# Kernel optimization log

Measured on AMD Instinct MI355X. Metric: run time of the kernel, lower is better.

The kernel has to match this reference:

```python
import jax, jax.numpy as jnp
import numpy as np

DIM = 2048
N_HEAD = 32
N_KV_HEAD = 8
HEAD_DIM = DIM // N_HEAD  # 64
BSZ = 2
SEQ = 2048


def apply_rotary_emb(x, freqs_cis):
    # x: [b, s, h, d]; freqs_cis: [s, d//2, 2]
    xs = x.reshape(*x.shape[:-1], -1, 2)          # [b, s, h, d//2, 2]
    fc = freqs_cis.reshape(1, xs.shape[1], 1, xs.shape[3], 2)
    x0, x1 = xs[..., 0], xs[..., 1]
    c, s = fc[..., 0], fc[..., 1]
    out = jnp.stack([x0 * c - x1 * s, x1 * c + x0 * s], axis=-1)
    return out.reshape(x.shape).astype(x.dtype)


def setup_inputs() -> dict:
    key = jax.random.key(0)
    k1, k2, k3, k4 = jax.random.split(key, 4)
    x = jax.random.normal(k1, (BSZ, SEQ, DIM), dtype=jnp.float32)
    # rotary cos/sin table [seq, head_dim//2, 2]
    theta = 1.0 / (10000.0 ** (jnp.arange(0, HEAD_DIM, 2, dtype=jnp.float32) / HEAD_DIM))
    ang = jnp.arange(SEQ, dtype=jnp.float32)[:, None] * theta[None, :]
    freqs_cis = jnp.stack([jnp.cos(ang), jnp.sin(ang)], axis=-1)
    mask = jnp.tril(jnp.ones((SEQ, SEQ), dtype=bool))  # causal
    scale = 0.02
    wqkv = jax.random.normal(k2, ((N_HEAD + 2 * N_KV_HEAD) * HEAD_DIM, DIM), dtype=jnp.float32) * scale
    wo = jax.random.normal(k3, (DIM, DIM), dtype=jnp.float32) * scale
    return {"x": x, "freqs_cis": freqs_cis, "mask": mask, "wqkv": wqkv, "wo": wo}


def reference(x, freqs_cis, mask, wqkv, wo):
    bsz, seqlen, _ = x.shape
    kv_size = N_KV_HEAD * HEAD_DIM
    qkv = x @ wqkv.T  # [b, s, dim + 2*kv]
    xq, xk, xv = jnp.split(qkv, [DIM, DIM + kv_size], axis=-1)
    xq = xq.reshape(bsz, seqlen, N_HEAD, HEAD_DIM)
    xk = xk.reshape(bsz, seqlen, N_KV_HEAD, HEAD_DIM)
    xv = xv.reshape(bsz, seqlen, N_KV_HEAD, HEAD_DIM)
    xq = apply_rotary_emb(xq, freqs_cis)
    xk = apply_rotary_emb(xk, freqs_cis)
    # [b, h, s, d]
    xq = xq.transpose(0, 2, 1, 3)
    xk = xk.transpose(0, 2, 1, 3)
    xv = xv.transpose(0, 2, 1, 3)
    rep = N_HEAD // N_KV_HEAD
    keys = jnp.repeat(xk, rep, axis=1)
    values = jnp.repeat(xv, rep, axis=1)
    scores = jnp.einsum("bhqd,bhkd->bhqk", xq, keys) / np.sqrt(HEAD_DIM).astype(np.float32)
    scores = jnp.where(mask, scores, jnp.finfo(scores.dtype).min)
    attn = jax.nn.softmax(scores, axis=-1)
    out = jnp.einsum("bhqk,bhkd->bhqd", attn, values)
    out = out.transpose(0, 2, 1, 3).reshape(bsz, seqlen, DIM)
    return out @ wo.T
```

## Files before the change

kernel.cpp:

```cpp
#include <hip/hip_runtime.h>
#include <hip/hip_bf16.h>

typedef __attribute__((ext_vector_type(8))) short short8;
typedef __attribute__((ext_vector_type(4))) short short4v;
typedef __attribute__((ext_vector_type(4))) float f32x4;
typedef __hip_bfloat16 bf16;

#define SEQ 2048
#define DIM 2048
#define NH 32
#define NKV 8
#define HD 64
#define QKVD 3072
#define KVD 512
#define SMSCALE 0.18033688011112042f

__device__ inline void gld_lds16(const bf16* g, bf16* l) {
    __builtin_amdgcn_global_load_lds((const __attribute__((address_space(1))) void*)g,
                                     (__attribute__((address_space(3))) void*)l, 16, 0, 0);
}

__device__ inline void store_val(float* p, float v) { *p = v; }
__device__ inline void store_val(bf16* p, float v) { *p = __float2bfloat16(v); }

__device__ inline unsigned pkbf16(float a, float b) {
    __hip_bfloat162 h = __float22bfloat162_rn(make_float2(a, b));
    return *(unsigned*)&h;
}

__global__ void cvt3_kernel(const float* __restrict__ x, const float* __restrict__ wqkv,
                            const float* __restrict__ wo, bf16* __restrict__ out) {
    int i = blockIdx.x * blockDim.x + threadIdx.x;
    const float* src; int off;
    if (i < 2097152) { src = x; off = i; }
    else if (i < 3670016) { src = wqkv; off = i - 2097152; }
    else { src = wo; off = i - 3670016; }
    float4 v = ((const float4*)src)[off];
    uint2 u;
    u.x = pkbf16(v.x, v.y);
    u.y = pkbf16(v.z, v.w);
    ((uint2*)out)[i] = u;
}

template <typename CT>
__global__ __launch_bounds__(256, 3) void gemm_nt(const bf16* __restrict__ A,
                                                  const bf16* __restrict__ Bt,
                                                  CT* __restrict__ C,
                                                  int M, int N, int K) {
    __shared__ bf16 As[128 * 32];
    __shared__ bf16 Bs[128 * 32];
    const int tid = threadIdx.x;
    const int lane = tid & 63;
    const int quad = lane >> 4;
    const int r16 = lane & 15;
    const int wave = tid >> 6;
    const int bm = blockIdx.y * 128;
    const int bn = blockIdx.x * 128;
    const int wm = (wave >> 1) * 64;
    const int wn = (wave & 1) * 64;

    f32x4 acc[4][4] = {};

    const int arow = tid >> 2;
    const int kch = (tid & 3) * 8;
    const bf16* Ap = A + (size_t)(bm + arow) * K + kch;
    const bf16* Bp = Bt + (size_t)(bn + arow) * K + kch;
    bf16* Asd = As + tid * 8;
    bf16* Bsd = Bs + tid * 8;
    const int kq = quad * 8;

    for (int k0 = 0; k0 < K; k0 += 32) {
        __syncthreads();
        gld_lds16(Ap, Asd);
        gld_lds16(Ap + (size_t)64 * K, Asd + 64 * 32);
        gld_lds16(Bp, Bsd);
        gld_lds16(Bp + (size_t)64 * K, Bsd + 64 * 32);
        Ap += 32; Bp += 32;
        __syncthreads();
        short8 af[4], bfr[4];
#pragma unroll
        for (int i = 0; i < 4; i++)
            af[i] = *(const short8*)(As + (wm + i * 16 + r16) * 32 + kq);
#pragma unroll
        for (int j = 0; j < 4; j++)
            bfr[j] = *(const short8*)(Bs + (wn + j * 16 + r16) * 32 + kq);
#pragma unroll
        for (int i = 0; i < 4; i++)
#pragma unroll
            for (int j = 0; j < 4; j++)
                acc[i][j] = __builtin_amdgcn_mfma_f32_16x16x32_bf16(af[i], bfr[j], acc[i][j], 0, 0, 0);
    }
#pragma unroll
    for (int i = 0; i < 4; i++)
#pragma unroll
        for (int j = 0; j < 4; j++) {
            int row = bm + wm + i * 16 + quad * 4;
            int col = bn + wn + j * 16 + r16;
#pragma unroll
            for (int r = 0; r < 4; r++)
                store_val(C + (size_t)(row + r) * N + col, acc[i][j][r]);
        }
}

__global__ void rope_qk_kernel(const bf16* __restrict__ qkv, const float* __restrict__ fc,
                               bf16* __restrict__ qr, bf16* __restrict__ kr) {
    int p = blockIdx.x * blockDim.x + threadIdx.x;
    int row = blockIdx.y;
    int s = row & (SEQ - 1);
    int b = row >> 11;
    int col = p * 2;
    const bf16* src = qkv + (size_t)row * QKVD + col;
    float x0 = __bfloat162float(src[0]);
    float x1 = __bfloat162float(src[1]);
    int j = (col & 63) >> 1;
    float c = fc[(s * 32 + j) * 2 + 0];
    float sn = fc[(s * 32 + j) * 2 + 1];
    if (col < DIM) {
        qr[(size_t)row * DIM + col]     = __float2bfloat16((x0 * c - x1 * sn) * SMSCALE);
        qr[(size_t)row * DIM + col + 1] = __float2bfloat16((x1 * c + x0 * sn) * SMSCALE);
    } else {
        int ck = col - DIM;
        kr[(size_t)row * KVD + ck]     = __float2bfloat16(x0 * c - x1 * sn);
        kr[(size_t)row * KVD + ck + 1] = __float2bfloat16(x1 * c + x0 * sn);
    }
    (void)b;
}

__global__ void rope_v_kernel(const bf16* __restrict__ qkv, bf16* __restrict__ vt) {
    const int t = threadIdx.x;
    const int so = t & 63;
    const int dq = t >> 6;
    const int bk = blockIdx.y;
    const int s = blockIdx.x * 64 + so;
    const int b = bk >> 3;
    const bf16* src = qkv + ((size_t)b * SEQ + s) * QKVD + DIM + KVD + (bk & 7) * HD + dq * 16;
    short8 v0 = *(const short8*)src;
    short8 v1 = *(const short8*)(src + 8);
    short* dst = (short*)(vt + ((size_t)bk * HD + dq * 16) * SEQ + s);
#pragma unroll
    for (int j = 0; j < 8; j++) dst[(size_t)j * SEQ] = v0[j];
#pragma unroll
    for (int j = 0; j < 8; j++) dst[(size_t)(8 + j) * SEQ] = v1[j];
}

__global__ __launch_bounds__(256, 5) void attn_kernel(const bf16* __restrict__ qr,
                                                      const bf16* __restrict__ kr,
                                                      const bf16* __restrict__ vt,
                                                      bf16* __restrict__ out) {
    __shared__ bf16 Ks[8192];
    __shared__ bf16 Vs[8192];
    const int t = threadIdx.x;
    const int lane = t & 63;
    const int wv = t >> 6;
    const int quad = lane >> 4;
    const int r16 = lane & 15;

    const int wg = blockIdx.x;
    const int xcd = wg & 7;
    const int kk = wg >> 3;
    const int bk = xcd * 2 + (kk & 1);
    const int qt = 127 - (kk >> 1);
    const int b = bk >> 3;
    const int kvh = bk & 7;
    const int h = kvh * 4 + wv;
    const int q0 = qt * 16;
    const int nkb = (qt >> 2) + 1;

    const bf16* Kg = kr + ((size_t)b * SEQ + lane) * KVD + kvh * HD + wv * 8;
    const bf16* Vg = vt + ((size_t)(b * NKV + kvh) * HD + lane) * SEQ + wv * 8;

    const char* kl = (const char*)Ks + quad * 1024 + r16 * 16;
    const char* vl = (const char*)Vs + (quad >> 1) * 1024 + r16 * 16 + (quad & 1) * 8;

    union PB { short4v s; unsigned u[2]; };

    const bf16* Qp = qr + ((size_t)b * SEQ + q0 + r16) * DIM + h * HD + quad * 8;
    short8 qa0 = *(const short8*)(Qp);
    short8 qa1 = *(const short8*)(Qp + 32);

    f32x4 o[4] = {};
    float l_i = 0.f;

    {
        bf16* Ksd = Ks + t * 8;
        bf16* Vsd = Vs + t * 8;
        gld_lds16(Kg, Ksd);      gld_lds16(Kg + 32, Ksd + 2048);
        gld_lds16(Vg, Vsd);      gld_lds16(Vg + 32, Vsd + 2048);
    }

    for (int kb = 0; kb < nkb; kb++) {
        __syncthreads();
        const int buf = kb & 1;
        if (kb + 1 < nkb) {
            const bf16* Kgn = Kg + (size_t)(kb + 1) * 64 * KVD;
            const bf16* Vgn = Vg + (kb + 1) * 64;
            bf16* Ksd = Ks + (buf ^ 1) * 4096 + t * 8;
            bf16* Vsd = Vs + (buf ^ 1) * 4096 + t * 8;
            gld_lds16(Kgn, Ksd);      gld_lds16(Kgn + 32, Ksd + 2048);
            gld_lds16(Vgn, Vsd);      gld_lds16(Vgn + 32, Vsd + 2048);
        }
        const char* klb = kl + buf * 8192;
        const char* vlb = vl + buf * 8192;

        const f32x4 z = {0.f, 0.f, 0.f, 0.f};
        f32x4 st[4];
        __builtin_amdgcn_s_setprio(1);
#pragma unroll
        for (int n = 0; n < 4; n++) {
            short8 kf0 = *(const short8*)(klb + n * 256);
            short8 kf1 = *(const short8*)(klb + 4096 + n * 256);
            st[n] = __builtin_amdgcn_mfma_f32_16x16x32_bf16(kf0, qa0, z, 0, 0, 0);
            st[n] = __builtin_amdgcn_mfma_f32_16x16x32_bf16(kf1, qa1, st[n], 0, 0, 0);
        }
        __builtin_amdgcn_s_setprio(0);
        short4v vf[4][4];
#pragma unroll
        for (int dt = 0; dt < 4; dt++)
#pragma unroll
            for (int n = 0; n < 4; n++)
                vf[dt][n] = *(const short4v*)(vlb + n * 2048 + dt * 256);

        if (kb == nkb - 1) {
            const int kbase = kb * 64;
#pragma unroll
            for (int n = 0; n < 4; n++)
#pragma unroll
                for (int r = 0; r < 4; r++) {
                    int key = kbase + n * 16 + quad * 4 + r;
                    if (key > q0 + r16) st[n][r] = -__builtin_inff();
                }
        }

        PB pbs[4];
#pragma unroll
        for (int n = 0; n < 4; n++) {
            float p0 = exp2f(st[n][0]);
            float p1 = exp2f(st[n][1]);
            float p2 = exp2f(st[n][2]);
            float p3 = exp2f(st[n][3]);
            l_i += (p0 + p1) + (p2 + p3);
            pbs[n].u[0] = pkbf16(p0, p1);
            pbs[n].u[1] = pkbf16(p2, p3);
        }

        __builtin_amdgcn_s_setprio(1);
#pragma unroll
        for (int dt = 0; dt < 4; dt++)
#pragma unroll
            for (int n = 0; n < 4; n++)
                o[dt] = __builtin_amdgcn_mfma_f32_16x16x16bf16_1k(vf[dt][n], pbs[n].s, o[dt], 0, 0, 0);
        __builtin_amdgcn_s_setprio(0);
    }

    float l = l_i;
    l += __shfl_xor(l, 16, 64);
    l += __shfl_xor(l, 32, 64);
    float inv_l = 1.f / l;
    bf16* Op = out + ((size_t)b * SEQ + q0 + r16) * DIM + h * HD + quad * 4;
#pragma unroll
    for (int dt = 0; dt < 4; dt++) {
        PB pk;
        pk.u[0] = pkbf16(o[dt][0] * inv_l, o[dt][1] * inv_l);
        pk.u[1] = pkbf16(o[dt][2] * inv_l, o[dt][3] * inv_l);
        *(short4v*)(Op + dt * 16) = pk.s;
    }
}

extern "C" void kernel_launch(void* const* d_in, const int* in_sizes, int n_in,
                              void* d_out, int out_size, void* d_ws, size_t ws_size,
                              hipStream_t stream) {
    (void)in_sizes; (void)n_in; (void)out_size; (void)ws_size;
    const float* x    = (const float*)d_in[0];
    const float* fc   = (const float*)d_in[1];
    const float* wqkv = (const float*)d_in[3];
    const float* wo   = (const float*)d_in[4];
    float* out = (float*)d_out;

    char* w = (char*)d_ws;
    bf16* xb    = (bf16*)(w);
    bf16* wqkvb = (bf16*)(w + 16777216);
    bf16* wob   = (bf16*)(w + 29360128);
    bf16* qkvb  = (bf16*)(w + 37748736);
    bf16* kr    = (bf16*)(w + 62914560);
    bf16* vt    = (bf16*)(w + 67108864);
    bf16* qr = xb;
    bf16* attnb = qkvb;

    cvt3_kernel<<<18432, 256, 0, stream>>>(x, wqkv, wo, xb);
    gemm_nt<bf16><<<dim3(24, 32), 256, 0, stream>>>(xb, wqkvb, qkvb, 4096, QKVD, DIM);
    rope_qk_kernel<<<dim3(5, 4096), 256, 0, stream>>>(qkvb, fc, qr, kr);
    rope_v_kernel<<<dim3(32, 16), 256, 0, stream>>>(qkvb, vt);
    attn_kernel<<<dim3(2048), 256, 0, stream>>>(qr, kr, vt, attnb);
    gemm_nt<float><<<dim3(16, 32), 256, 0, stream>>>(attnb, wob, out, 4096, DIM, DIM);
}
```

Baseline: 330.1 us.

## Vectorize RoPE kernel and compute softmax row sums via MFMA with ones

```diff
diff --git a/kernel.cpp b/kernel.cpp
--- a/kernel.cpp
+++ b/kernel.cpp
@@ -26,6 +26,11 @@
 __device__ inline unsigned pkbf16(float a, float b) {
     __hip_bfloat162 h = __float22bfloat162_rn(make_float2(a, b));
     return *(unsigned*)&h;
+}
+
+__device__ inline float b2f(short x) {
+    unsigned u = (unsigned)(unsigned short)x << 16;
+    union { unsigned u; float f; } c; c.u = u; return c.f;
 }
 
 __global__ void cvt3_kernel(const float* __restrict__ x, const float* __restrict__ wqkv,
@@ -104,26 +109,32 @@
 
 __global__ void rope_qk_kernel(const bf16* __restrict__ qkv, const float* __restrict__ fc,
                                bf16* __restrict__ qr, bf16* __restrict__ kr) {
-    int p = blockIdx.x * blockDim.x + threadIdx.x;
-    int row = blockIdx.y;
-    int s = row & (SEQ - 1);
-    int b = row >> 11;
-    int col = p * 2;
+    const int row = blockIdx.y;
+    const int s = row & (SEQ - 1);
+    const int col = (blockIdx.x * 64 + threadIdx.x) * 8;
     const bf16* src = qkv + (size_t)row * QKVD + col;
-    float x0 = __bfloat162float(src[0]);
-    float x1 = __bfloat162float(src[1]);
-    int j = (col & 63) >> 1;
-    float c = fc[(s * 32 + j) * 2 + 0];
-    float sn = fc[(s * 32 + j) * 2 + 1];
-    if (col < DIM) {
-        qr[(size_t)row * DIM + col]     = __float2bfloat16((x0 * c - x1 * sn) * SMSCALE);
-        qr[(size_t)row * DIM + col + 1] = __float2bfloat16((x1 * c + x0 * sn) * SMSCALE);
-    } else {
-        int ck = col - DIM;
-        kr[(size_t)row * KVD + ck]     = __float2bfloat16(x0 * c - x1 * sn);
-        kr[(size_t)row * KVD + ck + 1] = __float2bfloat16(x1 * c + x0 * sn);
-    }
-    (void)b;
+    short8 v = *(const short8*)src;
+    const int j0 = (col & 63) >> 1;
+    const float4* fcp = (const float4*)(fc + ((size_t)s * 32 + j0) * 2);
+    float4 f01 = fcp[0];
+    float4 f23 = fcp[1];
+
+    bf16* dst;
+    float sc;
+    if (col < DIM) { dst = qr + (size_t)row * DIM + col; sc = SMSCALE; }
+    else           { dst = kr + (size_t)row * KVD + (col - DIM); sc = 1.0f; }
+
+    float x0 = b2f(v[0]), x1 = b2f(v[1]), x2 = b2f(v[2]), x3 = b2f(v[3]);
+    float x4 = b2f(v[4]), x5 = b2f(v[5]), x6 = b2f(v[6]), x7 = b2f(v[7]);
+    float c0 = f01.x * sc, s0 = f01.y * sc, c1 = f01.z * sc, s1 = f01.w * sc;
+    float c2 = f23.x * sc, s2 = f23.y * sc, c3 = f23.z * sc, s3 = f23.w * sc;
+
+    uint4 o;
+    o.x = pkbf16(x0 * c0 - x1 * s0, x1 * c0 + x0 * s0);
+    o.y = pkbf16(x2 * c1 - x3 * s1, x3 * c1 + x2 * s1);
+    o.z = pkbf16(x4 * c2 - x5 * s2, x5 * c2 + x4 * s2);
+    o.w = pkbf16(x6 * c3 - x7 * s3, x7 * c3 + x6 * s3);
+    *(uint4*)dst = o;
 }
 
 __global__ void rope_v_kernel(const bf16* __restrict__ qkv, bf16* __restrict__ vt) {
@@ -143,7 +154,7 @@
     for (int j = 0; j < 8; j++) dst[(size_t)(8 + j) * SEQ] = v1[j];
 }
 
-__global__ __launch_bounds__(256, 5) void attn_kernel(const bf16* __restrict__ qr,
+__global__ __launch_bounds__(256, 4) void attn_kernel(const bf16* __restrict__ qr,
                                                       const bf16* __restrict__ kr,
                                                       const bf16* __restrict__ vt,
                                                       bf16* __restrict__ out) {
@@ -174,12 +185,15 @@
 
     union PB { short4v s; unsigned u[2]; };
 
+    const short one_bf16 = (short)0x3F80;
+    const short4v ones = {one_bf16, one_bf16, one_bf16, one_bf16};
+
     const bf16* Qp = qr + ((size_t)b * SEQ + q0 + r16) * DIM + h * HD + quad * 8;
     short8 qa0 = *(const short8*)(Qp);
     short8 qa1 = *(const short8*)(Qp + 32);
 
     f32x4 o[4] = {};
-    float l_i = 0.f;
+    f32x4 o_l = {};
 
     {
         bf16* Ksd = Ks + t * 8;
@@ -213,12 +227,14 @@
             st[n] = __builtin_amdgcn_mfma_f32_16x16x32_bf16(kf1, qa1, st[n], 0, 0, 0);
         }
         __builtin_amdgcn_s_setprio(0);
+
         short4v vf[4][4];
 #pragma unroll
         for (int dt = 0; dt < 4; dt++)
 #pragma unroll
             for (int n = 0; n < 4; n++)
                 vf[dt][n] = *(const short4v*)(vlb + n * 2048 + dt * 256);
+        __builtin_amdgcn_sched_barrier(0);
 
         if (kb == nkb - 1) {
             const int kbase = kb * 64;
@@ -238,7 +254,6 @@
             float p1 = exp2f(st[n][1]);
             float p2 = exp2f(st[n][2]);
             float p3 = exp2f(st[n][3]);
-            l_i += (p0 + p1) + (p2 + p3);
             pbs[n].u[0] = pkbf16(p0, p1);
             pbs[n].u[1] = pkbf16(p2, p3);
         }
@@ -249,13 +264,13 @@
 #pragma unroll
             for (int n = 0; n < 4; n++)
                 o[dt] = __builtin_amdgcn_mfma_f32_16x16x16bf16_1k(vf[dt][n], pbs[n].s, o[dt], 0, 0, 0);
+#pragma unroll
+        for (int n = 0; n < 4; n++)
+            o_l = __builtin_amdgcn_mfma_f32_16x16x16bf16_1k(ones, pbs[n].s, o_l, 0, 0, 0);
         __builtin_amdgcn_s_setprio(0);
     }
 
-    float l = l_i;
-    l += __shfl_xor(l, 16, 64);
-    l += __shfl_xor(l, 32, 64);
-    float inv_l = 1.f / l;
+    float inv_l = 1.f / o_l[0];
     bf16* Op = out + ((size_t)b * SEQ + q0 + r16) * DIM + h * HD + quad * 4;
 #pragma unroll
     for (int dt = 0; dt < 4; dt++) {
@@ -288,7 +303,7 @@
 
     cvt3_kernel<<<18432, 256, 0, stream>>>(x, wqkv, wo, xb);
     gemm_nt<bf16><<<dim3(24, 32), 256, 0, stream>>>(xb, wqkvb, qkvb, 4096, QKVD, DIM);
-    rope_qk_kernel<<<dim3(5, 4096), 256, 0, stream>>>(qkvb, fc, qr, kr);
+    rope_qk_kernel<<<dim3(5, 4096), 64, 0, stream>>>(qkvb, fc, qr, kr);
     rope_v_kernel<<<dim3(32, 16), 256, 0, stream>>>(qkvb, vt);
     attn_kernel<<<dim3(2048), 256, 0, stream>>>(qr, kr, vt, attnb);
     gemm_nt<float><<<dim3(16, 32), 256, 0, stream>>>(attnb, wob, out, 4096, DIM, DIM);
```

Result: no change. 326.2 us (-1.2%).
